# Performance work log

Measured on AMD Instinct MI355X. Metric: run time of the kernel, lower is better.

The kernel has to match this reference:

```python
import jax, jax.numpy as jnp
import numpy as np

B, N, OBS_DIM = 64, 512, 128
HIDDEN_DIM, MESSAGE_DIM, ACTION_DIM = 256, 128, 16


def _dense_params(key, din, dout):
    kw, kb = jax.random.split(key)
    W = jax.random.normal(kw, (din, dout), jnp.float32) * 0.02
    b = jnp.zeros((dout,), jnp.float32)
    return W, b


def setup_inputs() -> dict:
    key = jax.random.key(0)
    ks = jax.random.split(key, 12)
    obs_batch = jax.random.normal(ks[0], (B, N, OBS_DIM), jnp.float32)
    dones_batch = jnp.zeros((B, N), jnp.bool_)
    We, be = _dense_params(ks[1], OBS_DIM, HIDDEN_DIM)
    Wc, bc = _dense_params(ks[2], HIDDEN_DIM, MESSAGE_DIM // 4)
    Wn, bn = _dense_params(ks[3], HIDDEN_DIM, MESSAGE_DIM // 2)
    Wb, bb = _dense_params(ks[4], HIDDEN_DIM, MESSAGE_DIM // 4)
    Wi, bi = _dense_params(ks[5], HIDDEN_DIM, 1)
    Wq, bq = _dense_params(ks[6], HIDDEN_DIM, MESSAGE_DIM)
    Wk, bk = _dense_params(ks[7], MESSAGE_DIM, MESSAGE_DIM)
    Wv, bv = _dense_params(ks[8], MESSAGE_DIM, MESSAGE_DIM)
    Wp, bp = _dense_params(ks[9], HIDDEN_DIM + MESSAGE_DIM, HIDDEN_DIM)
    Wa, ba = _dense_params(ks[10], HIDDEN_DIM, ACTION_DIM)
    Wcr, bcr = _dense_params(ks[11], HIDDEN_DIM, 1)
    return {"obs_batch": obs_batch, "dones_batch": dones_batch,
            "We": We, "be": be, "Wc": Wc, "bc": bc, "Wn": Wn, "bn": bn,
            "Wb": Wb, "bb": bb, "Wi": Wi, "bi": bi, "Wq": Wq, "bq": bq,
            "Wk": Wk, "bk": bk, "Wv": Wv, "bv": bv, "Wp": Wp, "bp": bp,
            "Wa": Wa, "ba": ba, "Wcr": Wcr, "bcr": bcr}


def reference(obs_batch, dones_batch, We, be, Wc, bc, Wn, bn, Wb, bb, Wi, bi,
              Wq, bq, Wk, bk, Wv, bv, Wp, bp, Wa, ba, Wcr, bcr):
    dense = lambda x, W, b: x @ W + b
    encoded = jax.nn.relu(dense(obs_batch, We, be))                 # [B,N,H]
    messages = jnp.concatenate([dense(encoded, Wc, bc),
                                dense(encoded, Wn, bn),
                                dense(encoded, Wb, bb)], axis=-1)   # [B,N,M]
    importance = jax.nn.sigmoid(dense(encoded, Wi, bi))             # [B,N,1]
    Q = dense(encoded, Wq, bq)
    K = dense(messages, Wk, bk)
    V = dense(messages, Wv, bv)
    scores = jnp.einsum('bqd,bkd->bqk', Q, K) / jnp.sqrt(jnp.float32(MESSAGE_DIM))
    importance_weights = importance * jnp.transpose(importance, (0, 2, 1))  # [B,N,N]
    scores = scores * importance_weights
    norms = jnp.linalg.norm(obs_batch, axis=-1, keepdims=True)      # [B,N,1]
    obs_sim = jnp.einsum('bid,bjd->bij', obs_batch, obs_batch)
    obs_sim = obs_sim / (norms + 1e-08)
    obs_sim = obs_sim / (jnp.transpose(norms, (0, 2, 1)) + 1e-08)
    scores = scores + obs_sim * 0.5
    attn = jax.nn.softmax(scores, axis=-1)
    aggregated = jnp.einsum('bqk,bkd->bqd', attn, V)                # [B,N,M]
    combined = jnp.concatenate([encoded, aggregated], axis=-1)
    x = jax.nn.relu(dense(combined, Wp, bp))
    logits = dense(x, Wa, ba)
    value = dense(x, Wcr, bcr).squeeze(-1)
    return (logits, value)
```

## Files before the change

### kernel.cpp

```cpp
#include <hip/hip_runtime.h>
#include <math.h>


typedef __attribute__((ext_vector_type(8))) short short8;
typedef __attribute__((ext_vector_type(4))) float f32x4;

#define RSQRT_D 0.08838834764831843f
#define MFMA __builtin_amdgcn_mfma_f32_16x16x32_bf16

__device__ __forceinline__ unsigned short f2bf(float f) {
  union { float f; unsigned u; } v; v.f = f;
  return (unsigned short)((v.u + 0x7FFFu + ((v.u >> 16) & 1u)) >> 16);
}
__device__ __forceinline__ float bf2f(unsigned short h) {
  union { unsigned u; float f; } v; v.u = ((unsigned)h) << 16;
  return v.f;
}
__device__ __forceinline__ unsigned pack2(float a, float b) {
  return (unsigned)f2bf(a) | ((unsigned)f2bf(b) << 16);
}
__device__ __forceinline__ short8 ld8(const unsigned short* p) {
  return *(const short8*)p;
}
__device__ __forceinline__ void gl16(const unsigned short* g,
                                     unsigned short* l) {
  __builtin_amdgcn_global_load_lds(
      (const __attribute__((address_space(1))) unsigned int*)(const void*)g,
      (__attribute__((address_space(3))) unsigned int*)(void*)l, 16, 0, 0);
}

__global__ __launch_bounds__(256) void prep_all(
    const float* __restrict__ obs, const float* __restrict__ We,
    const float* __restrict__ Wq, const float* __restrict__ Wk,
    const float* __restrict__ Wv, const float* __restrict__ Wp,
    const float* __restrict__ Wc, const float* __restrict__ Wn,
    const float* __restrict__ Wb, const float* __restrict__ bc,
    const float* __restrict__ bn, const float* __restrict__ bb,
    const float* __restrict__ Wa, const float* __restrict__ Wcr,
    const float* __restrict__ ba, const float* __restrict__ bcr,
    const float* __restrict__ bq, unsigned short* __restrict__ WeT,
    unsigned short* __restrict__ Wqkv, unsigned short* __restrict__ Wkv,
    unsigned short* __restrict__ Wm_nt, unsigned short* __restrict__ WpT,
    unsigned short* __restrict__ WaCrT, float* __restrict__ bm,
    float* __restrict__ bqkv, unsigned short* __restrict__ obs_bf,
    unsigned short* __restrict__ As, unsigned short* __restrict__ Bs,
    float* __restrict__ logits, float* __restrict__ value,
    float* __restrict__ imp_raw) {
  const int bid = blockIdx.x, tid = threadIdx.x;
  if (bid < 929) {
    int idx = bid * 256 + tid;
    if (idx < 32768) {
      int n = idx >> 7, k = idx & 127;
      WeT[idx] = f2bf(We[k * 256 + n]);
    } else if (idx < 65536) {
      int i = idx - 32768;
      int n = i >> 8, k = i & 255;
      Wqkv[i] = f2bf(Wq[k * 128 + n]);
    } else if (idx < 98304) {
      int i = idx - 65536;
      int n = i >> 7, k = i & 127;
      Wkv[i] = f2bf(n < 128 ? Wk[k * 128 + n] : Wv[k * 128 + (n - 128)]);
    } else if (idx < 131072) {
      int i = idx - 98304;
      int h = i >> 7, m = i & 127;
      float v = (m < 32)   ? Wc[h * 32 + m]
              : (m < 96)   ? Wn[h * 64 + (m - 32)]
                           : Wb[h * 32 + (m - 96)];
      Wm_nt[i] = f2bf(v);
    } else if (idx < 229376) {
      int i = idx - 131072;
      int n = i / 384, k = i - n * 384;
      WpT[i] = f2bf(Wp[k * 256 + n]);
    } else if (idx < 237568) {
      int i = idx - 229376;
      int n = i >> 8, k = i & 255;
      float v = (n < 16) ? Wa[k * 16 + n] : (n == 16) ? Wcr[k] : 0.f;
      WaCrT[i] = f2bf(v);
    } else if (idx < 237696) {
      int i = idx - 237568;
      bm[i] = (i < 32) ? bc[i] : (i < 96) ? bn[i - 32] : bb[i - 96];
    } else if (idx < 237824) {
      int i = idx - 237696;
      bqkv[i] = bq[i];
    }
  } else if (bid < 2977) {
    const int wave = tid >> 6, lane = tid & 63;
    const int t0 = (bid - 929) * 16 + wave * 4;
#pragma unroll
    for (int it = 0; it < 4; ++it) {
      int t = t0 + it;
      const float* row = obs + (size_t)t * 128;
      float2 o = *(const float2*)(row + lane * 2);
      float s2 = o.x * o.x + o.y * o.y;
#pragma unroll
      for (int off = 1; off < 64; off <<= 1) s2 += __shfl_xor(s2, off);
      float inv = 1.f / (sqrtf(s2) + 1e-8f);
      ((unsigned*)obs_bf)[(size_t)t * 64 + lane] = pack2(o.x, o.y);
      ((unsigned*)As)[(size_t)t * 128 + 64 + lane] =
          pack2(o.x * 0.5f * inv, o.y * 0.5f * inv);
      ((unsigned*)Bs)[(size_t)t * 128 + 64 + lane] =
          pack2(o.x * inv, o.y * inv);
    }
  } else if (bid < 5153) {
    int i = (bid - 2977) * 256 + tid;
    if (i < 524288) logits[i] = ba[i & 15];
    else value[i - 524288] = bcr[0];
  } else {
    imp_raw[(bid - 5153) * 256 + tid] = 0.f;
  }
}

__global__ __launch_bounds__(256, 2) void enc_wprod(
    const unsigned short* __restrict__ obs_bf,
    const unsigned short* __restrict__ WeT, const float* __restrict__ be,
    const float* __restrict__ Wi, unsigned short* __restrict__ enc,
    float* __restrict__ imp_raw, const unsigned short* __restrict__ Wkv,
    const unsigned short* __restrict__ Wm_nt, const float* __restrict__ bmc,
    const float* __restrict__ bk, const float* __restrict__ bv,
    unsigned short* __restrict__ Wqkv, float* __restrict__ bqkv) {
  __shared__ unsigned short Asr[16384];
  __shared__ unsigned short Bsr[16384];
  const int bid = blockIdx.x, tid = threadIdx.x;

  if (bid >= 512) {
    const int wb = bid - 512;
    if (wb < 8) {
      const int lane = tid & 63, wave = tid >> 6;
      const int quad = lane >> 4, l16 = lane & 15;
      const int r0 = wb * 32;
      f32x4 acc[2][4];
#pragma unroll
      for (int i = 0; i < 2; ++i)
#pragma unroll
        for (int j = 0; j < 4; ++j) acc[i][j] = (f32x4){0.f, 0.f, 0.f, 0.f};
#pragma unroll
      for (int kc = 0; kc < 4; ++kc) {
        short8 af[2], bf[4];
#pragma unroll
        for (int i = 0; i < 2; ++i)
          af[i] =
              ld8(Wkv + (size_t)(r0 + i * 16 + l16) * 128 + kc * 32 + quad * 8);
#pragma unroll
        for (int j = 0; j < 4; ++j)
          bf[j] = ld8(Wm_nt + (size_t)(wave * 64 + j * 16 + l16) * 128 +
                      kc * 32 + quad * 8);
#pragma unroll
        for (int i = 0; i < 2; ++i)
#pragma unroll
          for (int j = 0; j < 4; ++j)
            acc[i][j] = MFMA(af[i], bf[j], acc[i][j], 0, 0, 0);
      }
#pragma unroll
      for (int i = 0; i < 2; ++i) {
        const int row = r0 + i * 16 + quad * 4;
#pragma unroll
        for (int j = 0; j < 4; ++j) {
          const int col = wave * 64 + j * 16 + l16;
#pragma unroll
          for (int r = 0; r < 4; ++r)
            Wqkv[(size_t)(128 + row + r) * 256 + col] = f2bf(acc[i][j][r]);
        }
      }
    } else {
      int i = tid;
      float acc = (i < 128) ? bk[i] : bv[i - 128];
      for (int m = 0; m < 128; ++m)
        acc += bmc[m] * bf2f(Wkv[(size_t)i * 128 + m]);
      bqkv[128 + i] = acc;
    }
    return;
  }

  const int lane = tid & 63, wave = tid >> 6;
  const int quad = lane >> 4, l16 = lane & 15;
  const int wm = wave & 1, wn = wave >> 1;
  const int bm0 = (bid >> 1) * 128, bn0 = (bid & 1) * 128;

#pragma unroll
  for (int it = 0; it < 8; ++it) {
    int c = it * 256 + tid;
    int row = c >> 4, ch = c & 15;
    gl16(obs_bf + (size_t)(bm0 + row) * 128 + ((ch ^ (row & 15)) << 3),
         Asr + it * 2048 + wave * 512);
    gl16(WeT + (size_t)(bn0 + row) * 128 + ((ch ^ (row & 15)) << 3),
         Bsr + it * 2048 + wave * 512);
  }
  __syncthreads();

  f32x4 acc[4][4];
#pragma unroll
  for (int i = 0; i < 4; ++i)
#pragma unroll
    for (int j = 0; j < 4; ++j) acc[i][j] = (f32x4){0.f, 0.f, 0.f, 0.f};
#pragma unroll
  for (int ks = 0; ks < 4; ++ks) {
    short8 af[4], bf[4];
#pragma unroll
    for (int mi = 0; mi < 4; ++mi) {
      int row = wm * 64 + mi * 16 + l16;
      af[mi] = *(const short8*)&Asr[row * 128 + (((ks * 4 + quad) ^ (row & 15)) << 3)];
    }
#pragma unroll
    for (int ni = 0; ni < 4; ++ni) {
      int row = wn * 64 + ni * 16 + l16;
      bf[ni] = *(const short8*)&Bsr[row * 128 + (((ks * 4 + quad) ^ (row & 15)) << 3)];
    }
#pragma unroll
    for (int mi = 0; mi < 4; ++mi)
#pragma unroll
      for (int ni = 0; ni < 4; ++ni)
        acc[mi][ni] = MFMA(af[mi], bf[ni], acc[mi][ni], 0, 0, 0);
  }

#pragma unroll
  for (int mi = 0; mi < 4; ++mi) {
    const int rowb = bm0 + wm * 64 + mi * 16 + quad * 4;
    float ip[4] = {0.f, 0.f, 0.f, 0.f};
#pragma unroll
    for (int ni = 0; ni < 4; ++ni) {
      const int col = bn0 + wn * 64 + ni * 16 + l16;
      const float bvv = be[col], wv = Wi[col];
#pragma unroll
      for (int r = 0; r < 4; ++r) {
        float v = fmaxf(acc[mi][ni][r] + bvv, 0.f);
        enc[(size_t)(rowb + r) * 256 + col] = f2bf(v);
        ip[r] += v * wv;
      }
    }
#pragma unroll
    for (int r = 0; r < 4; ++r) {
#pragma unroll
      for (int off = 1; off < 16; off <<= 1) ip[r] += __shfl_xor(ip[r], off);
    }
    if (l16 == 0) {
#pragma unroll
      for (int r = 0; r < 4; ++r) atomicAdd(&imp_raw[rowb + r], ip[r]);
    }
  }
}

__global__ __launch_bounds__(256, 2) void qkv_gemm(
    const unsigned short* __restrict__ enc, const unsigned short* __restrict__ Wqkv,
    const float* __restrict__ bqkv, const float* __restrict__ imp_raw,
    const float* __restrict__ bi, unsigned short* __restrict__ As,
    unsigned short* __restrict__ Bs, unsigned short* __restrict__ vT) {
  __shared__ unsigned short Asr[8192];
  __shared__ unsigned short Bsr[8192];
  const int tid = threadIdx.x, lane = tid & 63, wave = tid >> 6;
  const int quad = lane >> 4, l16 = lane & 15;
  const int wm = wave & 1, wn = wave >> 1;
  const int bx = blockIdx.x;
  const int bm0 = blockIdx.y * 128, bn0 = bx * 128;
  const int sr4 = tid >> 2, sl4 = tid & 3;

  f32x4 acc[4][4];
#pragma unroll
  for (int i = 0; i < 4; ++i)
#pragma unroll
    for (int j = 0; j < 4; ++j) acc[i][j] = (f32x4){0.f, 0.f, 0.f, 0.f};

  auto stage = [&](int t, int bo) {
#pragma unroll
    for (int i = 0; i < 2; ++i) {
      int row = i * 64 + sr4;
      int col = t * 32 + ((sl4 ^ (row & 3)) << 3);
      gl16(enc + (size_t)(bm0 + row) * 256 + col,
           Asr + bo + i * 2048 + wave * 512);
      gl16(Wqkv + (size_t)(bn0 + row) * 256 + col,
           Bsr + bo + i * 2048 + wave * 512);
    }
  };

  stage(0, 0);
  __syncthreads();
#pragma unroll 8
  for (int t = 0; t < 8; ++t) {
    if (t < 7) stage(t + 1, ((t + 1) & 1) * 4096);
    const int bo = (t & 1) * 4096;
    short8 af[4], bf[4];
#pragma unroll
    for (int mi = 0; mi < 4; ++mi) {
      int row = wm * 64 + mi * 16 + l16;
      af[mi] = *(const short8*)&Asr[bo + row * 32 + ((quad ^ (row & 3)) << 3)];
    }
#pragma unroll
    for (int ni = 0; ni < 4; ++ni) {
      int row = wn * 64 + ni * 16 + l16;
      bf[ni] = *(const short8*)&Bsr[bo + row * 32 + ((quad ^ (row & 3)) << 3)];
    }
#pragma unroll
    for (int mi = 0; mi < 4; ++mi)
#pragma unroll
      for (int ni = 0; ni < 4; ++ni)
        acc[mi][ni] = MFMA(af[mi], bf[ni], acc[mi][ni], 0, 0, 0);
    __syncthreads();
  }

  const float bi0 = bi[0];
#pragma unroll
  for (int mi = 0; mi < 4; ++mi) {
    const int rowb = bm0 + wm * 64 + mi * 16 + quad * 4;
    float sg[4];
    if (bx < 2) {
      const float mult = (bx == 0) ? RSQRT_D : 1.0f;
#pragma unroll
      for (int r = 0; r < 4; ++r)
        sg[r] = mult / (1.f + __expf(-(imp_raw[rowb + r] + bi0)));
    }
#pragma unroll
    for (int ni = 0; ni < 4; ++ni) {
      const int col = wn * 64 + ni * 16 + l16;
      const float bvv = bqkv[bx * 128 + col];
      if (bx == 0) {
#pragma unroll
        for (int r = 0; r < 4; ++r)
          As[(size_t)(rowb + r) * 256 + col] = f2bf((acc[mi][ni][r] + bvv) * sg[r]);
      } else if (bx == 1) {
#pragma unroll
        for (int r = 0; r < 4; ++r)
          Bs[(size_t)(rowb + r) * 256 + col] = f2bf((acc[mi][ni][r] + bvv) * sg[r]);
      } else {
        uint2 o;
        o.x = pack2(acc[mi][ni][0] + bvv, acc[mi][ni][1] + bvv);
        o.y = pack2(acc[mi][ni][2] + bvv, acc[mi][ni][3] + bvv);
        *(uint2*)(vT + ((size_t)(rowb >> 9) * 128 + col) * 512 + (rowb & 511)) = o;
      }
    }
  }
}

__global__ __launch_bounds__(512, 4) void flash4b(
    const unsigned short* __restrict__ As, const unsigned short* __restrict__ Bs,
    const unsigned short* __restrict__ vT, unsigned short* __restrict__ agg) {
  __shared__ unsigned short Ub[16384];
  __shared__ unsigned short Pp[8192];
  __shared__ float redm[2][64];
  __shared__ float reds[2][64];
  const int tid = threadIdx.x, lane = tid & 63, wave = tid >> 6;
  const int quad = lane >> 4, l16 = lane & 15;
  const int wm = wave & 3, wn = wave >> 2;
  const int b = blockIdx.x & 63;
  const int qt = blockIdx.x >> 6;
  const size_t tok0 = (size_t)b * 512 + qt * 64;
  const int srow = tid >> 4, slc = tid & 15;
  const int qr8 = tid >> 3, ql8 = tid & 7;

  short8 af[8];
#pragma unroll
  for (int kc = 0; kc < 8; ++kc)
    af[kc] = ld8(As + (tok0 + wm * 16 + l16) * 256 + kc * 32 + quad * 8);

  f32x4 s[4][4];
#pragma unroll
  for (int kt = 0; kt < 4; ++kt)
#pragma unroll
    for (int nt = 0; nt < 4; ++nt) s[kt][nt] = (f32x4){0.f, 0.f, 0.f, 0.f};

  auto qstage = [&](int c) {
    const int kt_ = c >> 2, dq_ = c & 3;
#pragma unroll
    for (int r2 = 0; r2 < 2; ++r2) {
      int row = r2 * 64 + qr8;
      gl16(Bs + ((size_t)b * 512 + kt_ * 128 + row) * 256 + dq_ * 64 +
               ((ql8 ^ (row & 7)) << 3),
           Ub + (c & 1) * 8192 + r2 * 4096 + wave * 512);
    }
  };
  qstage(0);
  __syncthreads();
#pragma unroll 16
  for (int c = 0; c < 16; ++c) {
    if (c < 15) qstage(c + 1);
    const int kt = c >> 2, dq = c & 3;
    const int ub0 = (c & 1) * 8192;
#pragma unroll
    for (int kk2 = 0; kk2 < 2; ++kk2) {
      short8 bfr[4];
#pragma unroll
      for (int nt = 0; nt < 4; ++nt) {
        int rr = wn * 64 + nt * 16 + l16;
        bfr[nt] = *(const short8*)&Ub[ub0 + rr * 64 +
                                      (((kk2 * 2 + quad) ^ (rr & 7)) << 3)];
      }
#pragma unroll
      for (int nt = 0; nt < 4; ++nt)
        s[kt][nt] = MFMA(af[dq * 2 + kk2], bfr[nt], s[kt][nt], 0, 0, 0);
    }
    __syncthreads();
  }

  const int rbase = wm * 16 + quad * 4;
  float mt[4];
#pragma unroll
  for (int r = 0; r < 4; ++r) {
    float mv = -1e30f;
#pragma unroll
    for (int kt = 0; kt < 4; ++kt)
#pragma unroll
      for (int nt = 0; nt < 4; ++nt) mv = fmaxf(mv, s[kt][nt][r]);
#pragma unroll
    for (int off = 1; off < 16; off <<= 1) mv = fmaxf(mv, __shfl_xor(mv, off));
    mt[r] = mv;
  }
  if (l16 == 0) {
#pragma unroll
    for (int r = 0; r < 4; ++r) redm[wn][rbase + r] = mt[r];
  }
  __syncthreads();
  float lsum[4];
#pragma unroll
  for (int r = 0; r < 4; ++r) {
    float mfull = fmaxf(mt[r], redm[1 ^ wn][rbase + r]);
    float sum = 0.f;
#pragma unroll
    for (int kt = 0; kt < 4; ++kt)
#pragma unroll
      for (int nt = 0; nt < 4; ++nt) {
        float p = __expf(s[kt][nt][r] - mfull);
        s[kt][nt][r] = p;
        sum += p;
      }
#pragma unroll
    for (int off = 1; off < 16; off <<= 1) sum += __shfl_xor(sum, off);
    lsum[r] = sum;
  }
  if (l16 == 0) {
#pragma unroll
    for (int r = 0; r < 4; ++r) reds[wn][rbase + r] = lsum[r];
  }
  __syncthreads();
  float linv[4];
#pragma unroll
  for (int r = 0; r < 4; ++r)
    linv[r] = 1.0f / (lsum[r] + reds[1 ^ wn][rbase + r]);

  f32x4 oacc[4];
#pragma unroll
  for (int nt = 0; nt < 4; ++nt) oacc[nt] = (f32x4){0.f, 0.f, 0.f, 0.f};
#pragma unroll
  for (int vt = 0; vt < 4; ++vt) {
    __syncthreads();
#pragma unroll
    for (int nt = 0; nt < 4; ++nt) {
      const int col = wn * 64 + nt * 16 + l16;
#pragma unroll
      for (int r = 0; r < 4; ++r) {
        const int row = rbase + r;
        Pp[row * 128 + (((col >> 3) ^ (row & 15)) << 3) + (col & 7)] =
            f2bf(s[vt][nt][r]);
      }
    }
#pragma unroll
    for (int i = 0; i < 4; ++i) {
      int row = i * 32 + srow;
      gl16(vT + ((size_t)b * 128 + row) * 512 + vt * 128 +
               ((slc ^ (row & 15)) << 3),
           Ub + i * 4096 + wave * 512);
    }
    __syncthreads();
#pragma unroll
    for (int kk = 0; kk < 4; ++kk) {
      const int prow = wm * 16 + l16;
      short8 pa = *(const short8*)&Pp[prow * 128 + (((kk * 4 + quad) ^ (prow & 15)) << 3)];
#pragma unroll
      for (int nt = 0; nt < 4; ++nt) {
        int rr = wn * 64 + nt * 16 + l16;
        short8 vb = *(const short8*)&Ub[rr * 128 + (((kk * 4 + quad) ^ (rr & 15)) << 3)];
        oacc[nt] = MFMA(pa, vb, oacc[nt], 0, 0, 0);
      }
    }
  }
#pragma unroll
  for (int nt = 0; nt < 4; ++nt) {
    const int col = wn * 64 + nt * 16 + l16;
#pragma unroll
    for (int r = 0; r < 4; ++r)
      agg[(tok0 + rbase + r) * 128 + col] = f2bf(oacc[nt][r] * linv[r]);
  }
}

__global__ __launch_bounds__(256, 2) void xh_gemm(
    const unsigned short* __restrict__ enc, const unsigned short* __restrict__ agg,
    const unsigned short* __restrict__ WpT, const float* __restrict__ bp,
    const unsigned short* __restrict__ WaCrT, float* __restrict__ logits,
    float* __restrict__ value) {
  __shared__ unsigned short sm[16384];
  unsigned short* Asr = sm;
  unsigned short* Bsr = sm + 8192;
  const int tid = threadIdx.x, lane = tid & 63, wave = tid >> 6;
  const int quad = lane >> 4, l16 = lane & 15;
  const int wm = wave & 1, wn = wave >> 1;
  const int bm = blockIdx.y * 128, bn = blockIdx.x * 128;
  const int sr4 = tid >> 2, sl4 = tid & 3;

  f32x4 acc[4][4];
#pragma unroll
  for (int i = 0; i < 4; ++i)
#pragma unroll
    for (int j = 0; j < 4; ++j) acc[i][j] = (f32x4){0.f, 0.f, 0.f, 0.f};

  auto stage = [&](int t, int bo) {
    const unsigned short* Ap;
    int lda, kc;
    if (t < 8) { Ap = enc; lda = 256; kc = t * 32; }
    else       { Ap = agg; lda = 128; kc = t * 32 - 256; }
#pragma unroll
    for (int i = 0; i < 2; ++i) {
      int row = i * 64 + sr4;
      int sw = (sl4 ^ (row & 3)) << 3;
      gl16(Ap + (size_t)(bm + row) * lda + kc + sw,
           Asr + bo + i * 2048 + wave * 512);
      gl16(WpT + (size_t)(bn + row) * 384 + t * 32 + sw,
           Bsr + bo + i * 2048 + wave * 512);
    }
  };

  stage(0, 0);
  __syncthreads();
#pragma unroll 12
  for (int t = 0; t < 12; ++t) {
    if (t < 11) stage(t + 1, ((t + 1) & 1) * 4096);
    const int bo = (t & 1) * 4096;
    short8 af[4], bf[4];
#pragma unroll
    for (int mi = 0; mi < 4; ++mi) {
      int row = wm * 64 + mi * 16 + l16;
      af[mi] = *(const short8*)&Asr[bo + row * 32 + ((quad ^ (row & 3)) << 3)];
    }
#pragma unroll
    for (int ni = 0; ni < 4; ++ni) {
      int row = wn * 64 + ni * 16 + l16;
      bf[ni] = *(const short8*)&Bsr[bo + row * 32 + ((quad ^ (row & 3)) << 3)];
    }
#pragma unroll
    for (int mi = 0; mi < 4; ++mi)
#pragma unroll
      for (int ni = 0; ni < 4; ++ni)
        acc[mi][ni] = MFMA(af[mi], bf[ni], acc[mi][ni], 0, 0, 0);
    __syncthreads();
  }

#pragma unroll
  for (int mi = 0; mi < 4; ++mi) {
    const int row = wm * 64 + mi * 16 + quad * 4;
#pragma unroll
    for (int ni = 0; ni < 4; ++ni) {
      const int colc = wn * 64 + ni * 16 + l16;
      const float bv = bp[bn + colc];
#pragma unroll
      for (int r = 0; r < 4; ++r) {
        float v = fmaxf(acc[mi][ni][r] + bv, 0.f);
        sm[(row + r) * 128 + (((colc >> 3) ^ ((row + r) & 15)) << 3) + (colc & 7)] =
            f2bf(v);
      }
    }
  }
  __syncthreads();

  f32x4 h[2][2];
#pragma unroll
  for (int i = 0; i < 2; ++i)
#pragma unroll
    for (int j = 0; j < 2; ++j) h[i][j] = (f32x4){0.f, 0.f, 0.f, 0.f};
#pragma unroll
  for (int kc = 0; kc < 4; ++kc) {
    short8 xa[2], wb[2];
#pragma unroll
    for (int hm = 0; hm < 2; ++hm) {
      int row = wave * 32 + hm * 16 + l16;
      xa[hm] = *(const short8*)&sm[row * 128 + (((kc * 4 + quad) ^ (row & 15)) << 3)];
    }
#pragma unroll
    for (int hn = 0; hn < 2; ++hn)
      wb[hn] = ld8(WaCrT + (size_t)(hn * 16 + l16) * 256 + bn + kc * 32 + quad * 8);
#pragma unroll
    for (int hm = 0; hm < 2; ++hm)
#pragma unroll
      for (int hn = 0; hn < 2; ++hn)
        h[hm][hn] = MFMA(xa[hm], wb[hn], h[hm][hn], 0, 0, 0);
  }
#pragma unroll
  for (int hm = 0; hm < 2; ++hm) {
#pragma unroll
    for (int hn = 0; hn < 2; ++hn) {
      const int n = hn * 16 + l16;
#pragma unroll
      for (int r = 0; r < 4; ++r) {
        const int grow = bm + wave * 32 + hm * 16 + quad * 4 + r;
        if (n < 16)
          atomicAdd(&logits[(size_t)grow * 16 + n], h[hm][hn][r]);
        else if (n == 16)
          atomicAdd(&value[grow], h[hm][hn][r]);
      }
    }
  }
}

extern "C" void kernel_launch(void* const* d_in, const int* in_sizes, int n_in,
                              void* d_out, int out_size, void* d_ws,
                              size_t ws_size, hipStream_t stream) {
  const float* obs = (const float*)d_in[0];
  const float* We = (const float*)d_in[2];
  const float* be = (const float*)d_in[3];
  const float* Wc = (const float*)d_in[4];
  const float* bc = (const float*)d_in[5];
  const float* Wn = (const float*)d_in[6];
  const float* bn = (const float*)d_in[7];
  const float* Wb = (const float*)d_in[8];
  const float* bb = (const float*)d_in[9];
  const float* Wi = (const float*)d_in[10];
  const float* bi = (const float*)d_in[11];
  const float* Wq = (const float*)d_in[12];
  const float* bq = (const float*)d_in[13];
  const float* Wk = (const float*)d_in[14];
  const float* bk = (const float*)d_in[15];
  const float* Wv = (const float*)d_in[16];
  const float* bv = (const float*)d_in[17];
  const float* Wp = (const float*)d_in[18];
  const float* bp = (const float*)d_in[19];
  const float* Wa = (const float*)d_in[20];
  const float* ba = (const float*)d_in[21];
  const float* Wcr = (const float*)d_in[22];
  const float* bcr = (const float*)d_in[23];

  char* base = (char*)d_ws;
  unsigned short* enc_bf = (unsigned short*)(base);
  unsigned short* As     = (unsigned short*)(base + 16777216);
  unsigned short* Bs     = (unsigned short*)(base + 33554432);
  unsigned short* obsagg = (unsigned short*)(base + 50331648);
  unsigned short* vT     = (unsigned short*)(base + 58720256);
  float* imp_raw         = (float*)(base + 67108864);
  unsigned short* WeT    = (unsigned short*)(base + 67239936);
  unsigned short* Wqkv   = (unsigned short*)(base + 67305472);
  unsigned short* Wkv    = (unsigned short*)(base + 67502080);
  unsigned short* Wm_nt  = (unsigned short*)(base + 67567616);
  unsigned short* WpT    = (unsigned short*)(base + 67633152);
  unsigned short* WaCrT  = (unsigned short*)(base + 67829760);
  float* bmb             = (float*)(base + 67846144);
  float* bqkv            = (float*)(base + 67846656);

  float* logits = (float*)d_out;
  float* value = (float*)d_out + 524288;

  prep_all<<<5281, 256, 0, stream>>>(obs, We, Wq, Wk, Wv, Wp, Wc, Wn, Wb, bc,
                                     bn, bb, Wa, Wcr, ba, bcr, bq, WeT, Wqkv,
                                     Wkv, Wm_nt, WpT, WaCrT, bmb, bqkv, obsagg,
                                     As, Bs, logits, value, imp_raw);
  enc_wprod<<<521, 256, 0, stream>>>(obsagg, WeT, be, Wi, enc_bf, imp_raw,
                                     Wkv, Wm_nt, bmb, bk, bv, Wqkv, bqkv);
  qkv_gemm<<<dim3(3, 256), 256, 0, stream>>>(enc_bf, Wqkv, bqkv, imp_raw, bi,
                                             As, Bs, vT);
  flash4b<<<512, 512, 0, stream>>>(As, Bs, vT, obsagg);
  xh_gemm<<<dim3(2, 256), 256, 0, stream>>>(enc_bf, obsagg, WpT, bp, WaCrT,
                                            logits, value);
}
```

Baseline: 183.9 us.

## Fuse encoder and QKV GEMMs into one kernel, move weight-product into prep

Merges the encoder GEMM and the QKV projection GEMM into a single kernel. Each block computes a 64-row encoded tile, keeps it in LDS, accumulates the importance logits in LDS instead of with global atomics, then streams Wqkv tiles through double-buffered LDS to produce Q, K and V directly. The Wk/Wv by message-weight product and the folded bias are moved into the prep kernel, reading fp32 weights directly. This removes one launch and the global round trip of the encoded activations for the QKV GEMM. In exchange, each block reloads the full WeT and Wqkv, and the large 80 KB LDS footprint limits how many blocks fit per CU.

```diff
diff --git a/kernel.cpp b/kernel.cpp
--- a/kernel.cpp
+++ b/kernel.cpp
@@ -38,16 +38,15 @@
     const float* __restrict__ bn, const float* __restrict__ bb,
     const float* __restrict__ Wa, const float* __restrict__ Wcr,
     const float* __restrict__ ba, const float* __restrict__ bcr,
-    const float* __restrict__ bq, unsigned short* __restrict__ WeT,
-    unsigned short* __restrict__ Wqkv, unsigned short* __restrict__ Wkv,
-    unsigned short* __restrict__ Wm_nt, unsigned short* __restrict__ WpT,
-    unsigned short* __restrict__ WaCrT, float* __restrict__ bm,
-    float* __restrict__ bqkv, unsigned short* __restrict__ obs_bf,
-    unsigned short* __restrict__ As, unsigned short* __restrict__ Bs,
-    float* __restrict__ logits, float* __restrict__ value,
-    float* __restrict__ imp_raw) {
+    const float* __restrict__ bq, const float* __restrict__ bk,
+    const float* __restrict__ bv, unsigned short* __restrict__ WeT,
+    unsigned short* __restrict__ Wqkv, unsigned short* __restrict__ WpT,
+    unsigned short* __restrict__ WaCrT, float* __restrict__ bqkv,
+    unsigned short* __restrict__ obs_bf, unsigned short* __restrict__ As,
+    unsigned short* __restrict__ Bs, float* __restrict__ logits,
+    float* __restrict__ value) {
   const int bid = blockIdx.x, tid = threadIdx.x;
-  if (bid < 929) {
+  if (bid < 673) {
     int idx = bid * 256 + tid;
     if (idx < 32768) {
       int n = idx >> 7, k = idx & 127;
@@ -56,36 +55,22 @@
       int i = idx - 32768;
       int n = i >> 8, k = i & 255;
       Wqkv[i] = f2bf(Wq[k * 128 + n]);
-    } else if (idx < 98304) {
+    } else if (idx < 163840) {
       int i = idx - 65536;
-      int n = i >> 7, k = i & 127;
-      Wkv[i] = f2bf(n < 128 ? Wk[k * 128 + n] : Wv[k * 128 + (n - 128)]);
-    } else if (idx < 131072) {
-      int i = idx - 98304;
-      int h = i >> 7, m = i & 127;
-      float v = (m < 32)   ? Wc[h * 32 + m]
-              : (m < 96)   ? Wn[h * 64 + (m - 32)]
-                           : Wb[h * 32 + (m - 96)];
-      Wm_nt[i] = f2bf(v);
-    } else if (idx < 229376) {
-      int i = idx - 131072;
       int n = i / 384, k = i - n * 384;
       WpT[i] = f2bf(Wp[k * 256 + n]);
-    } else if (idx < 237568) {
-      int i = idx - 229376;
+    } else if (idx < 172032) {
+      int i = idx - 163840;
       int n = i >> 8, k = i & 255;
       float v = (n < 16) ? Wa[k * 16 + n] : (n == 16) ? Wcr[k] : 0.f;
       WaCrT[i] = f2bf(v);
-    } else if (idx < 237696) {
-      int i = idx - 237568;
-      bm[i] = (i < 32) ? bc[i] : (i < 96) ? bn[i - 32] : bb[i - 96];
-    } else if (idx < 237824) {
-      int i = idx - 237696;
+    } else if (idx < 172160) {
+      int i = idx - 172032;
       bqkv[i] = bq[i];
     }
-  } else if (bid < 2977) {
+  } else if (bid < 2721) {
     const int wave = tid >> 6, lane = tid & 63;
-    const int t0 = (bid - 929) * 16 + wave * 4;
+    const int t0 = (bid - 673) * 16 + wave * 4;
 #pragma unroll
     for (int it = 0; it < 4; ++it) {
       int t = t0 + it;
@@ -101,88 +86,104 @@
       ((unsigned*)Bs)[(size_t)t * 128 + 64 + lane] =
           pack2(o.x * inv, o.y * inv);
     }
-  } else if (bid < 5153) {
-    int i = (bid - 2977) * 256 + tid;
+  } else if (bid < 4897) {
+    int i = (bid - 2721) * 256 + tid;
     if (i < 524288) logits[i] = ba[i & 15];
     else value[i - 524288] = bcr[0];
+  } else if (bid < 4905) {
+    const int wb = bid - 4897;
+    const int lane = tid & 63, wave = tid >> 6;
+    const int quad = lane >> 4, l16 = lane & 15;
+    const int r0 = wb * 32;
+    f32x4 acc[2][4];
+#pragma unroll
+    for (int i = 0; i < 2; ++i)
+#pragma unroll
+      for (int j = 0; j < 4; ++j) acc[i][j] = (f32x4){0.f, 0.f, 0.f, 0.f};
+#pragma unroll
+    for (int kc = 0; kc < 4; ++kc) {
+      short8 af[2], bf[4];
+#pragma unroll
+      for (int i = 0; i < 2; ++i) {
+        int n = r0 + i * 16 + l16;
+        const float* src = (n < 128) ? (Wk + n) : (Wv + (n - 128));
+        short8 v;
+#pragma unroll
+        for (int e = 0; e < 8; ++e)
+          v[e] = (short)f2bf(src[(size_t)(kc * 32 + quad * 8 + e) * 128]);
+        af[i] = v;
+      }
+#pragma unroll
+      for (int j = 0; j < 4; ++j) {
+        int h = wave * 64 + j * 16 + l16;
+        int m0 = kc * 32 + quad * 8;
+        const float* p = (m0 < 32)   ? (Wc + (size_t)h * 32 + m0)
+                       : (m0 < 96)   ? (Wn + (size_t)h * 64 + (m0 - 32))
+                                     : (Wb + (size_t)h * 32 + (m0 - 96));
+        short8 v;
+#pragma unroll
+        for (int e = 0; e < 8; ++e) v[e] = (short)f2bf(p[e]);
+        bf[j] = v;
+      }
+#pragma unroll
+      for (int i = 0; i < 2; ++i)
+#pragma unroll
+        for (int j = 0; j < 4; ++j)
+          acc[i][j] = MFMA(af[i], bf[j], acc[i][j], 0, 0, 0);
+    }
+#pragma unroll
+    for (int i = 0; i < 2; ++i) {
+      const int row = r0 + i * 16 + quad * 4;
+#pragma unroll
+      for (int j = 0; j < 4; ++j) {
+        const int col = wave * 64 + j * 16 + l16;
+#pragma unroll
+        for (int r = 0; r < 4; ++r)
+          Wqkv[(size_t)(128 + row + r) * 256 + col] = f2bf(acc[i][j][r]);
+      }
+    }
   } else {
-    imp_raw[(bid - 5153) * 256 + tid] = 0.f;
-  }
-}
-
-__global__ __launch_bounds__(256, 2) void enc_wprod(
+    int i = tid;
+    float acc = (i < 128) ? bk[i] : bv[i - 128];
+    for (int m = 0; m < 128; ++m) {
+      float bmv = (m < 32) ? bc[m] : (m < 96) ? bn[m - 32] : bb[m - 96];
+      float w = (i < 128) ? Wk[(size_t)m * 128 + i]
+                          : Wv[(size_t)m * 128 + (i - 128)];
+      acc += bmv * bf2f(f2bf(w));
+    }
+    bqkv[128 + i] = acc;
+  }
+}
+
+__global__ __launch_bounds__(256, 2) void encqkv(
     const unsigned short* __restrict__ obs_bf,
     const unsigned short* __restrict__ WeT, const float* __restrict__ be,
-    const float* __restrict__ Wi, unsigned short* __restrict__ enc,
-    float* __restrict__ imp_raw, const unsigned short* __restrict__ Wkv,
-    const unsigned short* __restrict__ Wm_nt, const float* __restrict__ bmc,
-    const float* __restrict__ bk, const float* __restrict__ bv,
-    unsigned short* __restrict__ Wqkv, float* __restrict__ bqkv) {
-  __shared__ unsigned short Asr[16384];
-  __shared__ unsigned short Bsr[16384];
-  const int bid = blockIdx.x, tid = threadIdx.x;
-
-  if (bid >= 512) {
-    const int wb = bid - 512;
-    if (wb < 8) {
-      const int lane = tid & 63, wave = tid >> 6;
-      const int quad = lane >> 4, l16 = lane & 15;
-      const int r0 = wb * 32;
-      f32x4 acc[2][4];
-#pragma unroll
-      for (int i = 0; i < 2; ++i)
-#pragma unroll
-        for (int j = 0; j < 4; ++j) acc[i][j] = (f32x4){0.f, 0.f, 0.f, 0.f};
-#pragma unroll
-      for (int kc = 0; kc < 4; ++kc) {
-        short8 af[2], bf[4];
-#pragma unroll
-        for (int i = 0; i < 2; ++i)
-          af[i] =
-              ld8(Wkv + (size_t)(r0 + i * 16 + l16) * 128 + kc * 32 + quad * 8);
-#pragma unroll
-        for (int j = 0; j < 4; ++j)
-          bf[j] = ld8(Wm_nt + (size_t)(wave * 64 + j * 16 + l16) * 128 +
-                      kc * 32 + quad * 8);
-#pragma unroll
-        for (int i = 0; i < 2; ++i)
-#pragma unroll
-          for (int j = 0; j < 4; ++j)
-            acc[i][j] = MFMA(af[i], bf[j], acc[i][j], 0, 0, 0);
-      }
-#pragma unroll
-      for (int i = 0; i < 2; ++i) {
-        const int row = r0 + i * 16 + quad * 4;
-#pragma unroll
-        for (int j = 0; j < 4; ++j) {
-          const int col = wave * 64 + j * 16 + l16;
-#pragma unroll
-          for (int r = 0; r < 4; ++r)
-            Wqkv[(size_t)(128 + row + r) * 256 + col] = f2bf(acc[i][j][r]);
-        }
-      }
-    } else {
-      int i = tid;
-      float acc = (i < 128) ? bk[i] : bv[i - 128];
-      for (int m = 0; m < 128; ++m)
-        acc += bmc[m] * bf2f(Wkv[(size_t)i * 128 + m]);
-      bqkv[128 + i] = acc;
-    }
-    return;
-  }
-
-  const int lane = tid & 63, wave = tid >> 6;
+    const float* __restrict__ Wi, const float* __restrict__ bi,
+    const unsigned short* __restrict__ Wqkv, const float* __restrict__ bqkv,
+    unsigned short* __restrict__ enc, unsigned short* __restrict__ As,
+    unsigned short* __restrict__ Bs, unsigned short* __restrict__ vT) {
+  __shared__ char smem[81920];
+  unsigned short* Asr = (unsigned short*)smem;
+  unsigned short* Bsr = (unsigned short*)(smem + 16384);
+  unsigned short* encl = (unsigned short*)smem;
+  unsigned short* Bq = (unsigned short*)(smem + 32768);
+  float* imp_lds = (float*)(smem + 65536);
+  const int tid = threadIdx.x, lane = tid & 63, wave = tid >> 6;
   const int quad = lane >> 4, l16 = lane & 15;
-  const int wm = wave & 1, wn = wave >> 1;
-  const int bm0 = (bid >> 1) * 128, bn0 = (bid & 1) * 128;
-
-#pragma unroll
-  for (int it = 0; it < 8; ++it) {
+  const int bm0 = blockIdx.x * 64;
+
+#pragma unroll
+  for (int it = 0; it < 4; ++it) {
     int c = it * 256 + tid;
     int row = c >> 4, ch = c & 15;
     gl16(obs_bf + (size_t)(bm0 + row) * 128 + ((ch ^ (row & 15)) << 3),
          Asr + it * 2048 + wave * 512);
-    gl16(WeT + (size_t)(bn0 + row) * 128 + ((ch ^ (row & 15)) << 3),
+  }
+#pragma unroll
+  for (int it = 0; it < 16; ++it) {
+    int c = it * 256 + tid;
+    int row = c >> 4, ch = c & 15;
+    gl16(WeT + (size_t)row * 128 + ((ch ^ (row & 15)) << 3),
          Bsr + it * 2048 + wave * 512);
   }
   __syncthreads();
@@ -197,12 +198,12 @@
     short8 af[4], bf[4];
 #pragma unroll
     for (int mi = 0; mi < 4; ++mi) {
-      int row = wm * 64 + mi * 16 + l16;
+      int row = mi * 16 + l16;
       af[mi] = *(const short8*)&Asr[row * 128 + (((ks * 4 + quad) ^ (row & 15)) << 3)];
     }
 #pragma unroll
     for (int ni = 0; ni < 4; ++ni) {
-      int row = wn * 64 + ni * 16 + l16;
+      int row = wave * 64 + ni * 16 + l16;
       bf[ni] = *(const short8*)&Bsr[row * 128 + (((ks * 4 + quad) ^ (row & 15)) << 3)];
     }
 #pragma unroll
@@ -211,19 +212,37 @@
       for (int ni = 0; ni < 4; ++ni)
         acc[mi][ni] = MFMA(af[mi], bf[ni], acc[mi][ni], 0, 0, 0);
   }
-
+  __syncthreads();
+
+  if (tid < 64) imp_lds[tid] = 0.f;
+  __syncthreads();
+
+  {
+#pragma unroll
+    for (int i = 0; i < 4; ++i) {
+      int row = i * 32 + (tid >> 3);
+      gl16(Wqkv + (size_t)row * 256 + (((tid & 7) ^ (row & 7)) << 3),
+           Bq + i * 2048 + wave * 512);
+    }
+  }
+
+  const float bi0 = bi[0];
 #pragma unroll
   for (int mi = 0; mi < 4; ++mi) {
-    const int rowb = bm0 + wm * 64 + mi * 16 + quad * 4;
+    const int rowl = mi * 16 + quad * 4;
     float ip[4] = {0.f, 0.f, 0.f, 0.f};
 #pragma unroll
     for (int ni = 0; ni < 4; ++ni) {
-      const int col = bn0 + wn * 64 + ni * 16 + l16;
+      const int col = wave * 64 + ni * 16 + l16;
       const float bvv = be[col], wv = Wi[col];
+      const int kh = col >> 7, ic = col & 127;
 #pragma unroll
       for (int r = 0; r < 4; ++r) {
+        const int row = rowl + r;
         float v = fmaxf(acc[mi][ni][r] + bvv, 0.f);
-        enc[(size_t)(rowb + r) * 256 + col] = f2bf(v);
+        enc[(size_t)(bm0 + row) * 256 + col] = f2bf(v);
+        encl[kh * 8192 + row * 128 + (((ic >> 3) ^ (row & 15)) << 3) + (ic & 7)] =
+            f2bf(v);
         ip[r] += v * wv;
       }
     }
@@ -234,96 +253,91 @@
     }
     if (l16 == 0) {
 #pragma unroll
-      for (int r = 0; r < 4; ++r) atomicAdd(&imp_raw[rowb + r], ip[r]);
-    }
-  }
-}
-
-__global__ __launch_bounds__(256, 2) void qkv_gemm(
-    const unsigned short* __restrict__ enc, const unsigned short* __restrict__ Wqkv,
-    const float* __restrict__ bqkv, const float* __restrict__ imp_raw,
-    const float* __restrict__ bi, unsigned short* __restrict__ As,
-    unsigned short* __restrict__ Bs, unsigned short* __restrict__ vT) {
-  __shared__ unsigned short Asr[8192];
-  __shared__ unsigned short Bsr[8192];
-  const int tid = threadIdx.x, lane = tid & 63, wave = tid >> 6;
-  const int quad = lane >> 4, l16 = lane & 15;
+      for (int r = 0; r < 4; ++r) atomicAdd(&imp_lds[rowl + r], ip[r]);
+    }
+  }
+  __syncthreads();
+
   const int wm = wave & 1, wn = wave >> 1;
-  const int bx = blockIdx.x;
-  const int bm0 = blockIdx.y * 128, bn0 = bx * 128;
-  const int sr4 = tid >> 2, sl4 = tid & 3;
-
-  f32x4 acc[4][4];
-#pragma unroll
-  for (int i = 0; i < 4; ++i)
-#pragma unroll
-    for (int j = 0; j < 4; ++j) acc[i][j] = (f32x4){0.f, 0.f, 0.f, 0.f};
-
-  auto stage = [&](int t, int bo) {
-#pragma unroll
-    for (int i = 0; i < 2; ++i) {
-      int row = i * 64 + sr4;
-      int col = t * 32 + ((sl4 ^ (row & 3)) << 3);
-      gl16(enc + (size_t)(bm0 + row) * 256 + col,
-           Asr + bo + i * 2048 + wave * 512);
-      gl16(Wqkv + (size_t)(bn0 + row) * 256 + col,
-           Bsr + bo + i * 2048 + wave * 512);
-    }
-  };
-
-  stage(0, 0);
-  __syncthreads();
-#pragma unroll 8
-  for (int t = 0; t < 8; ++t) {
-    if (t < 7) stage(t + 1, ((t + 1) & 1) * 4096);
-    const int bo = (t & 1) * 4096;
-    short8 af[4], bf[4];
-#pragma unroll
-    for (int mi = 0; mi < 4; ++mi) {
-      int row = wm * 64 + mi * 16 + l16;
-      af[mi] = *(const short8*)&Asr[bo + row * 32 + ((quad ^ (row & 3)) << 3)];
-    }
-#pragma unroll
-    for (int ni = 0; ni < 4; ++ni) {
-      int row = wn * 64 + ni * 16 + l16;
-      bf[ni] = *(const short8*)&Bsr[bo + row * 32 + ((quad ^ (row & 3)) << 3)];
-    }
-#pragma unroll
-    for (int mi = 0; mi < 4; ++mi)
-#pragma unroll
-      for (int ni = 0; ni < 4; ++ni)
-        acc[mi][ni] = MFMA(af[mi], bf[ni], acc[mi][ni], 0, 0, 0);
-    __syncthreads();
-  }
-
-  const float bi0 = bi[0];
-#pragma unroll
-  for (int mi = 0; mi < 4; ++mi) {
-    const int rowb = bm0 + wm * 64 + mi * 16 + quad * 4;
-    float sg[4];
-    if (bx < 2) {
-      const float mult = (bx == 0) ? RSQRT_D : 1.0f;
-#pragma unroll
-      for (int r = 0; r < 4; ++r)
-        sg[r] = mult / (1.f + __expf(-(imp_raw[rowb + r] + bi0)));
-    }
-#pragma unroll
-    for (int ni = 0; ni < 4; ++ni) {
-      const int col = wn * 64 + ni * 16 + l16;
-      const float bvv = bqkv[bx * 128 + col];
-      if (bx == 0) {
+  for (int ct = 0; ct < 3; ++ct) {
+    f32x4 a2[2][4];
+#pragma unroll
+    for (int i = 0; i < 2; ++i)
+#pragma unroll
+      for (int j = 0; j < 4; ++j) a2[i][j] = (f32x4){0.f, 0.f, 0.f, 0.f};
+#pragma unroll
+    for (int kt = 0; kt < 4; ++kt) {
+      if (kt < 3 || ct < 2) {
+        const int nct = (kt < 3) ? ct : ct + 1;
+        const int nkt = (kt < 3) ? kt + 1 : 0;
+        const int nbo = ((kt + 1) & 1) * 8192;
+#pragma unroll
+        for (int i = 0; i < 4; ++i) {
+          int row = i * 32 + (tid >> 3);
+          gl16(Wqkv + (size_t)(nct * 128 + row) * 256 + nkt * 64 +
+                   (((tid & 7) ^ (row & 7)) << 3),
+               Bq + nbo + i * 2048 + wave * 512);
+        }
+      }
+      const int bo = (kt & 1) * 8192;
+#pragma unroll
+      for (int ks2 = 0; ks2 < 2; ++ks2) {
+        const int kc = kt * 2 + ks2;
+        const int kh = kc >> 2, c4 = kc & 3;
+        short8 af2[2], bf2[4];
+#pragma unroll
+        for (int mi = 0; mi < 2; ++mi) {
+          int row = wm * 32 + mi * 16 + l16;
+          af2[mi] = *(const short8*)&encl[kh * 8192 + row * 128 +
+                                          (((c4 * 4 + quad) ^ (row & 15)) << 3)];
+        }
+#pragma unroll
+        for (int ni = 0; ni < 4; ++ni) {
+          int row = wn * 64 + ni * 16 + l16;
+          bf2[ni] = *(const short8*)&Bq[bo + row * 64 +
+                                        (((ks2 * 4 + quad) ^ (row & 7)) << 3)];
+        }
+#pragma unroll
+        for (int mi = 0; mi < 2; ++mi)
+#pragma unroll
+          for (int ni = 0; ni < 4; ++ni)
+            a2[mi][ni] = MFMA(af2[mi], bf2[ni], a2[mi][ni], 0, 0, 0);
+      }
+      __syncthreads();
+    }
+
+#pragma unroll
+    for (int mi = 0; mi < 2; ++mi) {
+      const int rowl = wm * 32 + mi * 16 + quad * 4;
+      const int rowb = bm0 + rowl;
+      float sg[4];
+      if (ct < 2) {
+        const float mult = (ct == 0) ? RSQRT_D : 1.0f;
 #pragma unroll
         for (int r = 0; r < 4; ++r)
-          As[(size_t)(rowb + r) * 256 + col] = f2bf((acc[mi][ni][r] + bvv) * sg[r]);
-      } else if (bx == 1) {
-#pragma unroll
-        for (int r = 0; r < 4; ++r)
-          Bs[(size_t)(rowb + r) * 256 + col] = f2bf((acc[mi][ni][r] + bvv) * sg[r]);
-      } else {
-        uint2 o;
-        o.x = pack2(acc[mi][ni][0] + bvv, acc[mi][ni][1] + bvv);
-        o.y = pack2(acc[mi][ni][2] + bvv, acc[mi][ni][3] + bvv);
-        *(uint2*)(vT + ((size_t)(rowb >> 9) * 128 + col) * 512 + (rowb & 511)) = o;
+          sg[r] = mult / (1.f + __expf(-(imp_lds[rowl + r] + bi0)));
+      }
+#pragma unroll
+      for (int ni = 0; ni < 4; ++ni) {
+        const int col = wn * 64 + ni * 16 + l16;
+        const float bvv = bqkv[ct * 128 + col];
+        if (ct == 0) {
+#pragma unroll
+          for (int r = 0; r < 4; ++r)
+            As[(size_t)(rowb + r) * 256 + col] =
+                f2bf((a2[mi][ni][r] + bvv) * sg[r]);
+        } else if (ct == 1) {
+#pragma unroll
+          for (int r = 0; r < 4; ++r)
+            Bs[(size_t)(rowb + r) * 256 + col] =
+                f2bf((a2[mi][ni][r] + bvv) * sg[r]);
+        } else {
+          uint2 o;
+          o.x = pack2(a2[mi][ni][0] + bvv, a2[mi][ni][1] + bvv);
+          o.y = pack2(a2[mi][ni][2] + bvv, a2[mi][ni][3] + bvv);
+          *(uint2*)(vT + ((size_t)(rowb >> 9) * 128 + col) * 512 +
+                    (rowb & 511)) = o;
+        }
       }
     }
   }
@@ -629,27 +643,21 @@
   unsigned short* Bs     = (unsigned short*)(base + 33554432);
   unsigned short* obsagg = (unsigned short*)(base + 50331648);
   unsigned short* vT     = (unsigned short*)(base + 58720256);
-  float* imp_raw         = (float*)(base + 67108864);
   unsigned short* WeT    = (unsigned short*)(base + 67239936);
   unsigned short* Wqkv   = (unsigned short*)(base + 67305472);
-  unsigned short* Wkv    = (unsigned short*)(base + 67502080);
-  unsigned short* Wm_nt  = (unsigned short*)(base + 67567616);
   unsigned short* WpT    = (unsigned short*)(base + 67633152);
   unsigned short* WaCrT  = (unsigned short*)(base + 67829760);
-  float* bmb             = (float*)(base + 67846144);
   float* bqkv            = (float*)(base + 67846656);
 
   float* logits = (float*)d_out;
   float* value = (float*)d_out + 524288;
 
-  prep_all<<<5281, 256, 0, stream>>>(obs, We, Wq, Wk, Wv, Wp, Wc, Wn, Wb, bc,
-                                     bn, bb, Wa, Wcr, ba, bcr, bq, WeT, Wqkv,
-                                     Wkv, Wm_nt, WpT, WaCrT, bmb, bqkv, obsagg,
-                                     As, Bs, logits, value, imp_raw);
-  enc_wprod<<<521, 256, 0, stream>>>(obsagg, WeT, be, Wi, enc_bf, imp_raw,
-                                     Wkv, Wm_nt, bmb, bk, bv, Wqkv, bqkv);
-  qkv_gemm<<<dim3(3, 256), 256, 0, stream>>>(enc_bf, Wqkv, bqkv, imp_raw, bi,
-                                             As, Bs, vT);
+  prep_all<<<4906, 256, 0, stream>>>(obs, We, Wq, Wk, Wv, Wp, Wc, Wn, Wb, bc,
+                                     bn, bb, Wa, Wcr, ba, bcr, bq, bk, bv, WeT,
+                                     Wqkv, WpT, WaCrT, bqkv, obsagg, As, Bs,
+                                     logits, value);
+  encqkv<<<512, 256, 0, stream>>>(obsagg, WeT, be, Wi, bi, Wqkv, bqkv, enc_bf,
+                                  As, Bs, vT);
   flash4b<<<512, 512, 0, stream>>>(As, Bs, vT, obsagg);
   xh_gemm<<<dim3(2, 256), 256, 0, stream>>>(enc_bf, obsagg, WpT, bp, WaCrT,
                                             logits, value);
```

Result: no change. 186.3 us (+1.3%).
